# Optimization experiments

Measured on AMD Instinct MI355X. Metric: run time of the kernel, lower is better.

Reference implementation:

```python
import jax, jax.numpy as jnp
import numpy as np

H = 4096       # hidden_size
NH = 32        # query heads
NKV = 2        # kv heads (multi_query_group_num)
HD = H // NH   # 128 head_dim
ROT = HD // 2  # GLM style: rotary applied to first half of head_dim
BASE = 10000.0
B, S = 2, 2048


def setup_inputs() -> dict:
    key = jax.random.key(0)
    k0, k1, k2, k3 = jax.random.split(key, 4)
    hidden_states = jax.random.normal(k0, (B, S, H), jnp.float32) * 0.02
    w_qkv = jax.random.normal(k1, (H, (NH + 2 * NKV) * HD), jnp.float32) * 0.02
    b_qkv = jax.random.normal(k2, ((NH + 2 * NKV) * HD,), jnp.float32) * 0.02
    w_dense = jax.random.normal(k3, (NH * HD, H), jnp.float32) * 0.02
    positions = jnp.broadcast_to(jnp.arange(S, dtype=jnp.int32), (B, S))
    return {"hidden_states": hidden_states, "w_qkv": w_qkv, "b_qkv": b_qkv,
            "w_dense": w_dense, "positions": positions}


def _glm_rope(x, positions):
    # x: [B, S, nheads, HD]; rotate first ROT dims, interleaved (non-neox) pairs
    inv_freq = 1.0 / (BASE ** (jnp.arange(0, ROT, 2, dtype=jnp.float32) / ROT))  # [ROT/2]
    ang = positions.astype(jnp.float32)[..., None] * inv_freq                     # [B,S,ROT/2]
    cos = jnp.cos(ang)[:, :, None, :]
    sin = jnp.sin(ang)[:, :, None, :]
    xr, xp = x[..., :ROT], x[..., ROT:]
    x1, x2 = xr[..., 0::2], xr[..., 1::2]
    o1 = x1 * cos - x2 * sin
    o2 = x1 * sin + x2 * cos
    rot = jnp.stack([o1, o2], axis=-1).reshape(xr.shape)
    return jnp.concatenate([rot, xp], axis=-1)


def reference(hidden_states, w_qkv, b_qkv, w_dense, positions):
    qkv = hidden_states @ w_qkv + b_qkv                       # [B,S,4608]
    q, k, v = jnp.split(qkv, [NH * HD, NH * HD + NKV * HD], axis=-1)
    q = q.reshape(B, S, NH, HD)
    k = k.reshape(B, S, NKV, HD)
    v = v.reshape(B, S, NKV, HD)
    q = _glm_rope(q, positions)
    k = _glm_rope(k, positions)
    # GQA: group query heads per kv head
    G = NH // NKV
    q = q.reshape(B, S, NKV, G, HD)
    scale = HD ** -0.5
    scores = jnp.einsum('bsgqd,btgd->bgqst', q, k) * scale    # [B,NKV,G,S,S]
    causal = jnp.tril(jnp.ones((S, S), dtype=bool))
    scores = jnp.where(causal, scores, jnp.finfo(scores.dtype).min)
    probs = jax.nn.softmax(scores, axis=-1)
    out = jnp.einsum('bgqst,btgd->bsgqd', probs, v)           # [B,S,NKV,G,HD]
    out = out.reshape(B, S, NH * HD)
    return out @ w_dense                                      # [B,S,H]
```

## Files before the change

kernel.cpp:

```cpp
#include <hip/hip_runtime.h>
#include <math.h>

#define B_    2
#define S_    2048
#define H_    4096
#define NH_   32
#define NKV_  2
#define HD_   128
#define ROT_  64
#define NQKV_ 4608
#define M_    4096
#define SCALE_ 0.088388347648318447f

typedef __attribute__((ext_vector_type(8))) short s16x8;
typedef __attribute__((ext_vector_type(4))) float f32x4;

__device__ __forceinline__ unsigned short f2bf(float x) {
  union { float f; unsigned u; } v; v.f = x;
  unsigned r = (v.u + 0x7fffu + ((v.u >> 16) & 1u)) >> 16;
  return (unsigned short)r;
}
__device__ __forceinline__ float bf2f(unsigned short u) {
  union { unsigned u; float f; } v; v.u = ((unsigned)u) << 16;
  return v.f;
}
__device__ __forceinline__ void gl_lds16(const unsigned short* g, unsigned short* l) {
  __builtin_amdgcn_global_load_lds(
      (const __attribute__((address_space(1))) void*)g,
      (__attribute__((address_space(3))) void*)l, 16, 0, 0);
}

__global__ __launch_bounds__(256) void cvt_bf16_kernel(
    const float* __restrict__ in, unsigned short* __restrict__ o, long n)
{
  long i = ((long)blockIdx.x * blockDim.x + threadIdx.x) * 8;
  if (i >= n) return;
  float4 a = *(const float4*)(in + i);
  float4 b = *(const float4*)(in + i + 4);
  s16x8 v;
  v[0] = f2bf(a.x); v[1] = f2bf(a.y); v[2] = f2bf(a.z); v[3] = f2bf(a.w);
  v[4] = f2bf(b.x); v[5] = f2bf(b.y); v[6] = f2bf(b.z); v[7] = f2bf(b.w);
  *(s16x8*)(o + i) = v;
}

__global__ __launch_bounds__(256) void wtrans_kernel(
    const float* __restrict__ w, unsigned short* __restrict__ wt, int K, int N)
{
  __shared__ __align__(16) unsigned short T[64][72];
  const int tid = threadIdx.x;
  const int k0 = blockIdx.x * 64;
  const int n0 = blockIdx.y * 64;

#pragma unroll
  for (int i = 0; i < 4; ++i) {
    int idx = tid + i * 256;
    int kr = idx >> 4;
    int nc = (idx & 15) << 2;
    float4 v = *(const float4*)(w + (size_t)(k0 + kr) * N + n0 + nc);
    T[nc + 0][kr] = f2bf(v.x);
    T[nc + 1][kr] = f2bf(v.y);
    T[nc + 2][kr] = f2bf(v.z);
    T[nc + 3][kr] = f2bf(v.w);
  }
  __syncthreads();
#pragma unroll
  for (int i = 0; i < 2; ++i) {
    int idx = tid + i * 256;
    int nr = idx >> 3;
    int kc = (idx & 7) << 3;
    s16x8 v = *(const s16x8*)&T[nr][kc];
    *(s16x8*)&wt[(size_t)(n0 + nr) * K + k0 + kc] = v;
  }
}

template<bool BF16OUT>
__global__ __launch_bounds__(256) void gemm_bf16_kernel(
    const unsigned short* __restrict__ A, const unsigned short* __restrict__ Bt,
    const float* __restrict__ bias, void* __restrict__ Cv,
    int M, int N, int K)
{
  __shared__ __align__(16) unsigned short As[128 * 32];
  __shared__ __align__(16) unsigned short Bs[128 * 32];
  const int tid  = threadIdx.x;
  const int lane = tid & 63;
  const int w    = tid >> 6;
  const int quad = lane >> 4;
  const int l15  = lane & 15;
  const int wm   = w >> 1;
  const int wn   = w & 1;
  const int bm = blockIdx.y * 128;
  const int bn = blockIdx.x * 128;

  const int r16 = lane >> 2;
  const int kc  = (lane & 3) << 3;
  const int c0  = w * 2;
  const unsigned short* Ag0 = A  + (size_t)(bm + (c0 + 0) * 16 + r16) * K + kc;
  const unsigned short* Ag1 = A  + (size_t)(bm + (c0 + 1) * 16 + r16) * K + kc;
  const unsigned short* Bg0 = Bt + (size_t)(bn + (c0 + 0) * 16 + r16) * K + kc;
  const unsigned short* Bg1 = Bt + (size_t)(bn + (c0 + 1) * 16 + r16) * K + kc;
  unsigned short* As0 = &As[(c0 + 0) * 512];
  unsigned short* As1 = &As[(c0 + 1) * 512];
  unsigned short* Bs0 = &Bs[(c0 + 0) * 512];
  unsigned short* Bs1 = &Bs[(c0 + 1) * 512];

  const unsigned short* Af = &As[(wm * 64 + l15) * 32 + (quad << 3)];
  const unsigned short* Bf = &Bs[(wn * 64 + l15) * 32 + (quad << 3)];

  f32x4 acc[4][4];
#pragma unroll
  for (int i = 0; i < 4; ++i)
#pragma unroll
    for (int j = 0; j < 4; ++j)
#pragma unroll
      for (int e = 0; e < 4; ++e) acc[i][j][e] = 0.0f;

  for (int k0 = 0; k0 < K; k0 += 32) {
    gl_lds16(Ag0 + k0, As0);
    gl_lds16(Ag1 + k0, As1);
    gl_lds16(Bg0 + k0, Bs0);
    gl_lds16(Bg1 + k0, Bs1);
    __syncthreads();
    s16x8 af[4], bfr[4];
#pragma unroll
    for (int mi = 0; mi < 4; ++mi) af[mi]  = *(const s16x8*)(Af + mi * 512);
#pragma unroll
    for (int ni = 0; ni < 4; ++ni) bfr[ni] = *(const s16x8*)(Bf + ni * 512);
#pragma unroll
    for (int mi = 0; mi < 4; ++mi)
#pragma unroll
      for (int ni = 0; ni < 4; ++ni)
        acc[mi][ni] = __builtin_amdgcn_mfma_f32_16x16x32_bf16(
            af[mi], bfr[ni], acc[mi][ni], 0, 0, 0);
    __syncthreads();
  }

  float bv[4];
#pragma unroll
  for (int ni = 0; ni < 4; ++ni)
    bv[ni] = bias ? bias[bn + wn * 64 + ni * 16 + l15] : 0.0f;

#pragma unroll
  for (int mi = 0; mi < 4; ++mi)
#pragma unroll
    for (int i = 0; i < 4; ++i) {
      size_t row = (size_t)(bm + wm * 64 + mi * 16 + (quad << 2) + i);
#pragma unroll
      for (int ni = 0; ni < 4; ++ni) {
        size_t idx = row * N + bn + wn * 64 + ni * 16 + l15;
        float val = acc[mi][ni][i] + bv[ni];
        if (BF16OUT) ((unsigned short*)Cv)[idx] = f2bf(val);
        else         ((float*)Cv)[idx] = val;
      }
    }
}

__global__ __launch_bounds__(256) void rope_kernel(
    unsigned short* __restrict__ qkv, const int* __restrict__ positions)
{
  int t = blockIdx.x * blockDim.x + threadIdx.x;
  const int total = M_ * (NH_ + NKV_) * (ROT_ / 2);
  if (t >= total) return;
  int pair = t & 31;
  int hh   = (t >> 5) % (NH_ + NKV_);
  int tok  = t / (32 * (NH_ + NKV_));
  int col  = hh * HD_;
  float pos  = (float)positions[tok];
  float freq = powf(10000.0f, -(float)pair * (1.0f / 32.0f));
  float ang  = pos * freq;
  float s = sinf(ang), c = cosf(ang);
  size_t base = (size_t)tok * NQKV_ + col + 2 * pair;
  unsigned v = *(const unsigned*)(qkv + base);
  float x1 = bf2f((unsigned short)(v & 0xffffu));
  float x2 = bf2f((unsigned short)(v >> 16));
  float o1 = x1 * c - x2 * s;
  float o2 = x1 * s + x2 * c;
  *(unsigned*)(qkv + base) = (unsigned)f2bf(o1) | ((unsigned)f2bf(o2) << 16);
}

__global__ __launch_bounds__(256) void vtrans_kernel(
    const unsigned short* __restrict__ qkv, unsigned short* __restrict__ vt)
{
  __shared__ __align__(16) unsigned short T[64][72];
  const int tid = threadIdx.x;
  const int s0 = blockIdx.x * 64;
  const int c0 = blockIdx.y * 64;
  const int bg = blockIdx.z;
  const int b = bg >> 1, g = bg & 1;

#pragma unroll
  for (int i = 0; i < 2; ++i) {
    int idx = tid + i * 256;
    int sr = idx >> 3;
    int cc = (idx & 7) << 3;
    const unsigned short* p = qkv + (size_t)(b * S_ + s0 + sr) * NQKV_
                     + (NH_ + NKV_) * HD_ + g * HD_ + c0 + cc;
    s16x8 v = *(const s16x8*)p;
#pragma unroll
    for (int j = 0; j < 8; ++j) T[cc + j][sr] = (unsigned short)v[j];
  }
  __syncthreads();
#pragma unroll
  for (int i = 0; i < 2; ++i) {
    int idx = tid + i * 256;
    int cr = idx >> 3;
    int kc = idx & 7;
    s16x8 v = *(const s16x8*)&T[cr][kc << 3];
    *(s16x8*)&vt[(size_t)((bg << 7) + c0 + cr) * S_ + s0 + (kc << 3)] = v;
  }
}

#define QS_OFF 8704
#define VT_OFF 8704
#define PS_OFF 16896

__global__ __launch_bounds__(256) void flash_mfma_kernel(
    const unsigned short* __restrict__ qkv, const unsigned short* __restrict__ vt,
    unsigned short* __restrict__ out)
{
  __shared__ __align__(16) unsigned short smem[21504];

  const int tid  = threadIdx.x;
  const int lane = tid & 63;
  const int w    = tid >> 6;
  const int quad = lane >> 4;
  const int l15  = lane & 15;
  const int q0 = blockIdx.x * 64;
  const int b  = blockIdx.y >> 5;
  const int h  = blockIdx.y & 31;
  const int g  = h >> 4;
  const int bg = b * NKV_ + g;
  const size_t tok0 = (size_t)b * S_;

#pragma unroll
  for (int i = 0; i < 4; ++i) {
    int idx = tid + i * 256;
    int r = idx >> 4, c8 = (idx & 15) << 3;
    s16x8 v = *(const s16x8*)(qkv + (tok0 + q0 + r) * NQKV_ + h * HD_ + c8);
    *(s16x8*)&smem[QS_OFF + r * 136 + c8] = v;
  }
  __syncthreads();

  s16x8 qf[4];
#pragma unroll
  for (int ks = 0; ks < 4; ++ks)
    qf[ks] = *(const s16x8*)&smem[QS_OFF + (w * 16 + l15) * 136 + (quad << 3) + (ks << 5)];
  __syncthreads();

  f32x4 O[8];
#pragma unroll
  for (int n = 0; n < 8; ++n)
#pragma unroll
    for (int i = 0; i < 4; ++i) O[n][i] = 0.0f;
  float m_i[4] = {-INFINITY, -INFINITY, -INFINITY, -INFINITY};
  float l_i[4] = {0.f, 0.f, 0.f, 0.f};

  for (int kt = 0; kt <= q0; kt += 64) {
#pragma unroll
    for (int i = 0; i < 4; ++i) {
      int idx = tid + i * 256;
      int key = idx >> 4, c8 = (idx & 15) << 3;
      s16x8 v = *(const s16x8*)(qkv + (tok0 + kt + key) * NQKV_ + NH_ * HD_ + g * HD_ + c8);
      *(s16x8*)&smem[key * 136 + c8] = v;
    }
#pragma unroll
    for (int i = 0; i < 4; ++i) {
      int idx = tid + i * 256;
      int c = idx >> 3, kc = idx & 7;
      s16x8 v = *(const s16x8*)&vt[(size_t)((bg << 7) + c) * S_ + kt + (kc << 3)];
      *(s16x8*)&smem[VT_OFF + (c << 6) + (((kc + c) & 7) << 3)] = v;
    }
    __syncthreads();

    f32x4 S[4];
#pragma unroll
    for (int nt = 0; nt < 4; ++nt) {
#pragma unroll
      for (int i = 0; i < 4; ++i) S[nt][i] = 0.0f;
#pragma unroll
      for (int ks = 0; ks < 4; ++ks) {
        s16x8 kf = *(const s16x8*)&smem[(nt * 16 + l15) * 136 + (quad << 3) + (ks << 5)];
        S[nt] = __builtin_amdgcn_mfma_f32_16x16x32_bf16(qf[ks], kf, S[nt], 0, 0, 0);
      }
#pragma unroll
      for (int i = 0; i < 4; ++i) S[nt][i] *= SCALE_;
    }

    if (kt == q0) {
#pragma unroll
      for (int nt = 0; nt < 4; ++nt) {
        int colL = nt * 16 + l15;
#pragma unroll
        for (int i = 0; i < 4; ++i) {
          int rowL = w * 16 + quad * 4 + i;
          if (colL > rowL) S[nt][i] = -INFINITY;
        }
      }
    }

    float mx[4], alpha[4], rs[4];
#pragma unroll
    for (int i = 0; i < 4; ++i) {
      mx[i] = fmaxf(fmaxf(S[0][i], S[1][i]), fmaxf(S[2][i], S[3][i]));
#pragma unroll
      for (int off = 1; off < 16; off <<= 1)
        mx[i] = fmaxf(mx[i], __shfl_xor(mx[i], off));
      float mn = fmaxf(m_i[i], mx[i]);
      alpha[i] = __expf(m_i[i] - mn);
      m_i[i] = mn;
      rs[i] = 0.0f;
    }
#pragma unroll
    for (int nt = 0; nt < 4; ++nt)
#pragma unroll
      for (int i = 0; i < 4; ++i) {
        float p = __expf(S[nt][i] - m_i[i]);
        S[nt][i] = p;
        rs[i] += p;
      }
#pragma unroll
    for (int i = 0; i < 4; ++i) {
#pragma unroll
      for (int off = 1; off < 16; off <<= 1)
        rs[i] += __shfl_xor(rs[i], off);
      l_i[i] = l_i[i] * alpha[i] + rs[i];
    }

#pragma unroll
    for (int nt = 0; nt < 4; ++nt)
#pragma unroll
      for (int i = 0; i < 4; ++i)
        smem[PS_OFF + (w * 16 + quad * 4 + i) * 72 + nt * 16 + l15] = f2bf(S[nt][i]);

#pragma unroll
    for (int n = 0; n < 8; ++n)
#pragma unroll
      for (int i = 0; i < 4; ++i) O[n][i] *= alpha[i];

    __syncthreads();

    s16x8 pf[2];
#pragma unroll
    for (int ks2 = 0; ks2 < 2; ++ks2)
      pf[ks2] = *(const s16x8*)&smem[PS_OFF + (w * 16 + l15) * 72 + (quad << 3) + (ks2 << 5)];
#pragma unroll
    for (int nt2 = 0; nt2 < 8; ++nt2) {
      int col = nt2 * 16 + l15;
#pragma unroll
      for (int ks2 = 0; ks2 < 2; ++ks2) {
        int kc = ks2 * 4 + quad;
        s16x8 vf = *(const s16x8*)&smem[VT_OFF + (col << 6) + (((kc + col) & 7) << 3)];
        O[nt2] = __builtin_amdgcn_mfma_f32_16x16x32_bf16(pf[ks2], vf, O[nt2], 0, 0, 0);
      }
    }
    __syncthreads();
  }

  float inv[4];
#pragma unroll
  for (int i = 0; i < 4; ++i) inv[i] = 1.0f / l_i[i];
#pragma unroll
  for (int nt2 = 0; nt2 < 8; ++nt2)
#pragma unroll
    for (int i = 0; i < 4; ++i) {
      size_t row = tok0 + q0 + w * 16 + quad * 4 + i;
      out[row * H_ + h * HD_ + nt2 * 16 + l15] = f2bf(O[nt2][i] * inv[i]);
    }
}

extern "C" void kernel_launch(void* const* d_in, const int* in_sizes, int n_in,
                              void* d_out, int out_size, void* d_ws, size_t ws_size,
                              hipStream_t stream)
{
  (void)in_sizes; (void)n_in; (void)out_size; (void)ws_size;
  const float* hidden    = (const float*)d_in[0];
  const float* w_qkv     = (const float*)d_in[1];
  const float* b_qkv     = (const float*)d_in[2];
  const float* w_dense   = (const float*)d_in[3];
  const int*   positions = (const int*)d_in[4];
  float* out = (float*)d_out;

  unsigned short* hbf   = (unsigned short*)d_ws;
  unsigned short* wqkvT = (unsigned short*)((char*)d_ws + 33554432);
  unsigned short* vtb   = (unsigned short*)d_ws;
  unsigned short* abf   = (unsigned short*)((char*)d_ws + 2097152);
  unsigned short* wdT   = (unsigned short*)((char*)d_ws + 35651584);
  unsigned short* qkvb  = (unsigned short*)d_out;

  cvt_bf16_kernel<<<8192, 256, 0, stream>>>(hidden, hbf, (long)M_ * H_);
  wtrans_kernel<<<dim3(H_ / 64, NQKV_ / 64), 256, 0, stream>>>(w_qkv, wqkvT, H_, NQKV_);

  gemm_bf16_kernel<true><<<dim3(NQKV_ / 128, M_ / 128), 256, 0, stream>>>(
      hbf, wqkvT, b_qkv, qkvb, M_, NQKV_, H_);

  {
    int total = M_ * (NH_ + NKV_) * (ROT_ / 2);
    rope_kernel<<<(total + 255) / 256, 256, 0, stream>>>(qkvb, positions);
  }

  vtrans_kernel<<<dim3(S_ / 64, HD_ / 64, B_ * NKV_), 256, 0, stream>>>(qkvb, vtb);
  wtrans_kernel<<<dim3(H_ / 64, H_ / 64), 256, 0, stream>>>(w_dense, wdT, H_, H_);

  flash_mfma_kernel<<<dim3(S_ / 64, B_ * NH_), 256, 0, stream>>>(qkvb, vtb, abf);

  gemm_bf16_kernel<false><<<dim3(H_ / 128, M_ / 128), 256, 0, stream>>>(
      abf, wdT, nullptr, out, M_, H_, H_);
}
```

Measured before the change: 984.4 us.

## Process two 64-row query tiles per flash-attention block to reuse K/V tiles

Each flash-attention block now handles 128 query rows (two 64-row sub-tiles per wave) instead of 64, so every K and V tile loaded into shared memory feeds twice as many MFMAs. This halves global K/V traffic and per-tile sync overhead relative to compute. In exchange, register use per thread roughly doubles (two O accumulators, two softmax states), the grid shrinks by half, and the causal mask is now applied per sub-tile with global indices, with some fully-masked work on the last tile for the first sub-tile.

```diff
diff --git a/kernel.cpp b/kernel.cpp
--- a/kernel.cpp
+++ b/kernel.cpp
@@ -209,52 +209,59 @@
   }
 }
 
-#define QS_OFF 8704
 #define VT_OFF 8704
 #define PS_OFF 16896
 
-__global__ __launch_bounds__(256) void flash_mfma_kernel(
+__global__ __launch_bounds__(256, 2) void flash_mfma_kernel(
     const unsigned short* __restrict__ qkv, const unsigned short* __restrict__ vt,
     unsigned short* __restrict__ out)
 {
-  __shared__ __align__(16) unsigned short smem[21504];
+  __shared__ __align__(16) unsigned short smem[26112];
 
   const int tid  = threadIdx.x;
   const int lane = tid & 63;
   const int w    = tid >> 6;
   const int quad = lane >> 4;
   const int l15  = lane & 15;
-  const int q0 = blockIdx.x * 64;
+  const int q0 = blockIdx.x * 128;
   const int b  = blockIdx.y >> 5;
   const int h  = blockIdx.y & 31;
   const int g  = h >> 4;
   const int bg = b * NKV_ + g;
   const size_t tok0 = (size_t)b * S_;
 
-#pragma unroll
-  for (int i = 0; i < 4; ++i) {
-    int idx = tid + i * 256;
-    int r = idx >> 4, c8 = (idx & 15) << 3;
-    s16x8 v = *(const s16x8*)(qkv + (tok0 + q0 + r) * NQKV_ + h * HD_ + c8);
-    *(s16x8*)&smem[QS_OFF + r * 136 + c8] = v;
-  }
-  __syncthreads();
-
-  s16x8 qf[4];
-#pragma unroll
-  for (int ks = 0; ks < 4; ++ks)
-    qf[ks] = *(const s16x8*)&smem[QS_OFF + (w * 16 + l15) * 136 + (quad << 3) + (ks << 5)];
-  __syncthreads();
-
-  f32x4 O[8];
-#pragma unroll
-  for (int n = 0; n < 8; ++n)
-#pragma unroll
-    for (int i = 0; i < 4; ++i) O[n][i] = 0.0f;
-  float m_i[4] = {-INFINITY, -INFINITY, -INFINITY, -INFINITY};
-  float l_i[4] = {0.f, 0.f, 0.f, 0.f};
-
-  for (int kt = 0; kt <= q0; kt += 64) {
+  s16x8 qf[2][4];
+#pragma unroll
+  for (int mt = 0; mt < 2; ++mt) {
+#pragma unroll
+    for (int i = 0; i < 4; ++i) {
+      int idx = tid + i * 256;
+      int r = idx >> 4, c8 = (idx & 15) << 3;
+      s16x8 v = *(const s16x8*)(qkv + (tok0 + q0 + mt * 64 + r) * NQKV_ + h * HD_ + c8);
+      *(s16x8*)&smem[r * 136 + c8] = v;
+    }
+    __syncthreads();
+#pragma unroll
+    for (int ks = 0; ks < 4; ++ks)
+      qf[mt][ks] = *(const s16x8*)&smem[(w * 16 + l15) * 136 + (quad << 3) + (ks << 5)];
+    __syncthreads();
+  }
+
+  f32x4 O[2][8];
+#pragma unroll
+  for (int mt = 0; mt < 2; ++mt)
+#pragma unroll
+    for (int n = 0; n < 8; ++n)
+#pragma unroll
+      for (int i = 0; i < 4; ++i) O[mt][n][i] = 0.0f;
+  float m_i[2][4], l_i[2][4];
+#pragma unroll
+  for (int mt = 0; mt < 2; ++mt)
+#pragma unroll
+    for (int i = 0; i < 4; ++i) { m_i[mt][i] = -INFINITY; l_i[mt][i] = 0.f; }
+
+  const int ktend = q0 + 64;
+  for (int kt = 0; kt <= ktend; kt += 64) {
 #pragma unroll
     for (int i = 0; i < 4; ++i) {
       int idx = tid + i * 256;
@@ -271,77 +278,96 @@
     }
     __syncthreads();
 
-    f32x4 S[4];
+    f32x4 S[2][4];
+#pragma unroll
+    for (int mt = 0; mt < 2; ++mt)
+#pragma unroll
+      for (int nt = 0; nt < 4; ++nt)
+#pragma unroll
+        for (int i = 0; i < 4; ++i) S[mt][nt][i] = 0.0f;
 #pragma unroll
     for (int nt = 0; nt < 4; ++nt) {
-#pragma unroll
-      for (int i = 0; i < 4; ++i) S[nt][i] = 0.0f;
 #pragma unroll
       for (int ks = 0; ks < 4; ++ks) {
         s16x8 kf = *(const s16x8*)&smem[(nt * 16 + l15) * 136 + (quad << 3) + (ks << 5)];
-        S[nt] = __builtin_amdgcn_mfma_f32_16x16x32_bf16(qf[ks], kf, S[nt], 0, 0, 0);
-      }
-#pragma unroll
-      for (int i = 0; i < 4; ++i) S[nt][i] *= SCALE_;
-    }
-
-    if (kt == q0) {
-#pragma unroll
-      for (int nt = 0; nt < 4; ++nt) {
-        int colL = nt * 16 + l15;
+#pragma unroll
+        for (int mt = 0; mt < 2; ++mt)
+          S[mt][nt] = __builtin_amdgcn_mfma_f32_16x16x32_bf16(qf[mt][ks], kf, S[mt][nt], 0, 0, 0);
+      }
+#pragma unroll
+      for (int mt = 0; mt < 2; ++mt)
+#pragma unroll
+        for (int i = 0; i < 4; ++i) S[mt][nt][i] *= SCALE_;
+    }
+
+#pragma unroll
+    for (int mt = 0; mt < 2; ++mt) {
+      if (kt >= q0 + mt * 64) {
+#pragma unroll
+        for (int nt = 0; nt < 4; ++nt) {
+          int colG = kt + nt * 16 + l15;
+#pragma unroll
+          for (int i = 0; i < 4; ++i) {
+            int rowG = q0 + mt * 64 + w * 16 + quad * 4 + i;
+            if (colG > rowG) S[mt][nt][i] = -INFINITY;
+          }
+        }
+      }
+    }
+
+    float alpha[2][4];
+#pragma unroll
+    for (int mt = 0; mt < 2; ++mt) {
+      float mx[4], rs[4];
+#pragma unroll
+      for (int i = 0; i < 4; ++i) {
+        mx[i] = fmaxf(fmaxf(S[mt][0][i], S[mt][1][i]), fmaxf(S[mt][2][i], S[mt][3][i]));
+#pragma unroll
+        for (int off = 1; off < 16; off <<= 1)
+          mx[i] = fmaxf(mx[i], __shfl_xor(mx[i], off));
+        float mn = fmaxf(m_i[mt][i], mx[i]);
+        alpha[mt][i] = __expf(m_i[mt][i] - mn);
+        m_i[mt][i] = mn;
+        rs[i] = 0.0f;
+      }
+#pragma unroll
+      for (int nt = 0; nt < 4; ++nt)
 #pragma unroll
         for (int i = 0; i < 4; ++i) {
-          int rowL = w * 16 + quad * 4 + i;
-          if (colL > rowL) S[nt][i] = -INFINITY;
+          float p = __expf(S[mt][nt][i] - m_i[mt][i]);
+          S[mt][nt][i] = p;
+          rs[i] += p;
         }
-      }
-    }
-
-    float mx[4], alpha[4], rs[4];
-#pragma unroll
-    for (int i = 0; i < 4; ++i) {
-      mx[i] = fmaxf(fmaxf(S[0][i], S[1][i]), fmaxf(S[2][i], S[3][i]));
-#pragma unroll
-      for (int off = 1; off < 16; off <<= 1)
-        mx[i] = fmaxf(mx[i], __shfl_xor(mx[i], off));
-      float mn = fmaxf(m_i[i], mx[i]);
-      alpha[i] = __expf(m_i[i] - mn);
-      m_i[i] = mn;
-      rs[i] = 0.0f;
-    }
-#pragma unroll
-    for (int nt = 0; nt < 4; ++nt)
 #pragma unroll
       for (int i = 0; i < 4; ++i) {
-        float p = __expf(S[nt][i] - m_i[i]);
-        S[nt][i] = p;
-        rs[i] += p;
-      }
-#pragma unroll
-    for (int i = 0; i < 4; ++i) {
-#pragma unroll
-      for (int off = 1; off < 16; off <<= 1)
-        rs[i] += __shfl_xor(rs[i], off);
-      l_i[i] = l_i[i] * alpha[i] + rs[i];
-    }
-
-#pragma unroll
-    for (int nt = 0; nt < 4; ++nt)
-#pragma unroll
-      for (int i = 0; i < 4; ++i)
-        smem[PS_OFF + (w * 16 + quad * 4 + i) * 72 + nt * 16 + l15] = f2bf(S[nt][i]);
-
-#pragma unroll
-    for (int n = 0; n < 8; ++n)
-#pragma unroll
-      for (int i = 0; i < 4; ++i) O[n][i] *= alpha[i];
-
-    __syncthreads();
-
-    s16x8 pf[2];
-#pragma unroll
-    for (int ks2 = 0; ks2 < 2; ++ks2)
-      pf[ks2] = *(const s16x8*)&smem[PS_OFF + (w * 16 + l15) * 72 + (quad << 3) + (ks2 << 5)];
+#pragma unroll
+        for (int off = 1; off < 16; off <<= 1)
+          rs[i] += __shfl_xor(rs[i], off);
+        l_i[mt][i] = l_i[mt][i] * alpha[mt][i] + rs[i];
+      }
+
+#pragma unroll
+      for (int nt = 0; nt < 4; ++nt)
+#pragma unroll
+        for (int i = 0; i < 4; ++i)
+          smem[PS_OFF + (mt * 64 + w * 16 + quad * 4 + i) * 72 + nt * 16 + l15]
+              = f2bf(S[mt][nt][i]);
+
+#pragma unroll
+      for (int n = 0; n < 8; ++n)
+#pragma unroll
+        for (int i = 0; i < 4; ++i) O[mt][n][i] *= alpha[mt][i];
+    }
+
+    __syncthreads();
+
+    s16x8 pf[2][2];
+#pragma unroll
+    for (int mt = 0; mt < 2; ++mt)
+#pragma unroll
+      for (int ks2 = 0; ks2 < 2; ++ks2)
+        pf[mt][ks2] = *(const s16x8*)&smem[PS_OFF + (mt * 64 + w * 16 + l15) * 72
+                                           + (quad << 3) + (ks2 << 5)];
 #pragma unroll
     for (int nt2 = 0; nt2 < 8; ++nt2) {
       int col = nt2 * 16 + l15;
@@ -349,22 +375,27 @@
       for (int ks2 = 0; ks2 < 2; ++ks2) {
         int kc = ks2 * 4 + quad;
         s16x8 vf = *(const s16x8*)&smem[VT_OFF + (col << 6) + (((kc + col) & 7) << 3)];
-        O[nt2] = __builtin_amdgcn_mfma_f32_16x16x32_bf16(pf[ks2], vf, O[nt2], 0, 0, 0);
-      }
-    }
-    __syncthreads();
-  }
-
-  float inv[4];
-#pragma unroll
-  for (int i = 0; i < 4; ++i) inv[i] = 1.0f / l_i[i];
-#pragma unroll
-  for (int nt2 = 0; nt2 < 8; ++nt2)
-#pragma unroll
-    for (int i = 0; i < 4; ++i) {
-      size_t row = tok0 + q0 + w * 16 + quad * 4 + i;
-      out[row * H_ + h * HD_ + nt2 * 16 + l15] = f2bf(O[nt2][i] * inv[i]);
-    }
+#pragma unroll
+        for (int mt = 0; mt < 2; ++mt)
+          O[mt][nt2] = __builtin_amdgcn_mfma_f32_16x16x32_bf16(pf[mt][ks2], vf, O[mt][nt2], 0, 0, 0);
+      }
+    }
+    __syncthreads();
+  }
+
+#pragma unroll
+  for (int mt = 0; mt < 2; ++mt) {
+    float inv[4];
+#pragma unroll
+    for (int i = 0; i < 4; ++i) inv[i] = 1.0f / l_i[mt][i];
+#pragma unroll
+    for (int nt2 = 0; nt2 < 8; ++nt2)
+#pragma unroll
+      for (int i = 0; i < 4; ++i) {
+        size_t row = tok0 + q0 + mt * 64 + w * 16 + quad * 4 + i;
+        out[row * H_ + h * HD_ + nt2 * 16 + l15] = f2bf(O[mt][nt2][i] * inv[i]);
+      }
+  }
 }
 
 extern "C" void kernel_launch(void* const* d_in, const int* in_sizes, int n_in,
@@ -400,7 +431,7 @@
   vtrans_kernel<<<dim3(S_ / 64, HD_ / 64, B_ * NKV_), 256, 0, stream>>>(qkvb, vtb);
   wtrans_kernel<<<dim3(H_ / 64, H_ / 64), 256, 0, stream>>>(w_dense, wdT, H_, H_);
 
-  flash_mfma_kernel<<<dim3(S_ / 64, B_ * NH_), 256, 0, stream>>>(qkvb, vtb, abf);
+  flash_mfma_kernel<<<dim3(S_ / 128, B_ * NH_), 256, 0, stream>>>(qkvb, vtb, abf);
 
   gemm_bf16_kernel<false><<<dim3(H_ / 128, M_ / 128), 256, 0, stream>>>(
       abf, wdT, nullptr, out, M_, H_, H_);
```

After: 922.5 us. -6.3%, faster.
